# Performance work log

Measured on AMD Instinct MI355X. Metric: run time of the kernel, lower is better.

The kernel has to match this reference:

```python
import jax, jax.numpy as jnp
import numpy as np

CHANNELS = 256
CODEBOOK_SIZE = 8192
UPDATE_SPEED = 0.01
N_TOKENS = 32768


def setup_inputs() -> dict:
    key = jax.random.key(0)
    k1, k2 = jax.random.split(key)
    embeddings = jax.random.normal(k1, (N_TOKENS, CHANNELS), dtype=jnp.float32)
    code_usage = jnp.ones((CODEBOOK_SIZE,), dtype=jnp.float32)
    code_embedding_sum = jax.random.normal(k2, (CODEBOOK_SIZE, CHANNELS), dtype=jnp.float32)
    return {"embeddings": embeddings, "code_usage": code_usage,
            "code_embedding_sum": code_embedding_sum}


def reference(embeddings, code_usage, code_embedding_sum):
    # codebook from EMA statistics: [K, C]
    codebook = code_embedding_sum / jnp.clip(code_usage, 1e-5, None)[:, None]

    # encode: nearest code by Euclidean distance. argmin over codes is
    # invariant under sqrt, so use squared distances (avoids sqrt of [K, N]).
    cb_sq = jnp.sum(codebook * codebook, axis=-1)            # [K]
    x_sq = jnp.sum(embeddings * embeddings, axis=-1)         # [N]
    # d2[k, n] = ||cb_k - x_n||^2
    d2 = cb_sq[:, None] - 2.0 * jnp.einsum('kc,nc->kn', codebook, embeddings) + x_sq[None, :]
    codes = jnp.argmin(d2, axis=0).astype(jnp.int32)         # [N]

    # decode: gather codebook rows
    quantized = jnp.take(codebook, codes, axis=0)            # [N, C]

    # straight-through estimator
    embeddings_q = embeddings + jax.lax.stop_gradient(quantized - embeddings)

    # commitment loss: mse(stop_grad(embeddings_q), embeddings)
    diff = jax.lax.stop_gradient(embeddings_q) - embeddings
    commitment_loss = jnp.mean(diff * diff)

    # EMA updates (training mode, under no_grad in the original)
    n = embeddings.shape[0]
    counts = jax.ops.segment_sum(jnp.ones((n,), dtype=code_usage.dtype),
                                 codes, num_segments=CODEBOOK_SIZE)
    emb_sum = jax.ops.segment_sum(embeddings, codes, num_segments=CODEBOOK_SIZE)
    s = jnp.float32(UPDATE_SPEED)
    new_code_usage = jax.lax.stop_gradient(code_usage * (1.0 - s) + counts * s)
    new_code_embedding_sum = jax.lax.stop_gradient(
        code_embedding_sum * (1.0 - s) + emb_sum * s)

    return codes, embeddings_q, commitment_loss, new_code_usage, new_code_embedding_sum
```

## Files before the change

### kernel.cpp

```cpp
#include <hip/hip_runtime.h>

#define CH 256
#define KC 8192
#define NT 32768

#define TPW 32
#define JT  64
#define JTS 64

typedef _Float16 half4_t __attribute__((ext_vector_type(4)));
typedef _Float16 half8_t __attribute__((ext_vector_type(8)));
typedef float floatx16 __attribute__((ext_vector_type(16)));

typedef __attribute__((address_space(1))) const unsigned int guint_t;
typedef __attribute__((address_space(3))) unsigned int luint_t;

__global__ void k_prep(const float* __restrict__ usage,
                       const float* __restrict__ ces,
                       const float* __restrict__ emb,
                       _Float16* __restrict__ cbh,
                       _Float16* __restrict__ cbl,
                       float* __restrict__ cbsq,
                       _Float16* __restrict__ eh,
                       _Float16* __restrict__ el,
                       int* __restrict__ hist,
                       unsigned long long* __restrict__ packed) {
    int b = blockIdx.x, t = threadIdx.x;
    if (b < KC) {
        float uc = fmaxf(usage[b], 1e-5f);
        float v  = ces[b * CH + t];
        float cb = v / uc;
        _Float16 h = (_Float16)cb;
        cbh[b * CH + t] = h;
        cbl[b * CH + t] = (_Float16)(cb - (float)h);

        float p = cb * cb;
        #pragma unroll
        for (int off = 32; off; off >>= 1) p += __shfl_down(p, off);
        __shared__ float ps[4];
        int lane = t & 63, w = t >> 6;
        if (lane == 0) ps[w] = p;
        __syncthreads();
        if (t == 0) cbsq[b] = ps[0] + ps[1] + ps[2] + ps[3];
        if (t == 1) hist[b] = 0;
        int gid = b * CH + t;
        if (gid < NT) packed[gid] = 0xFFFFFFFFFFFFFFFFull;
    } else {
        int i = (b - KC) * 256 + t;
        float4 v = ((const float4*)emb)[i];
        float va[4] = {v.x, v.y, v.z, v.w};
        half4_t h, l;
        #pragma unroll
        for (int q = 0; q < 4; ++q) {
            _Float16 hh = (_Float16)va[q];
            h[q] = hh;
            l[q] = (_Float16)(va[q] - (float)hh);
        }
        ((half4_t*)eh)[i] = h;
        ((half4_t*)el)[i] = l;
    }
}

__launch_bounds__(512, 2)
__global__ void k_argmin(const _Float16* __restrict__ eh,
                         const _Float16* __restrict__ el,
                         const _Float16* __restrict__ cbh,
                         const _Float16* __restrict__ cbl,
                         const float* __restrict__ cbsq,
                         unsigned long long* __restrict__ packed) {
    __shared__ __align__(16) char smB[131072];

    const int t    = threadIdx.x;
    const int lane = t & 63;
    const int wave = t >> 6;
    const int lr32 = lane & 31;
    const int kh   = lane >> 5;

    const int n0w = blockIdx.x * 256 + wave * TPW;
    const int jq  = blockIdx.y * (JTS * JT);

    half8_t aregh[16], aregl[16];
    {
        const size_t rowoff = (size_t)(n0w + lr32) * CH + kh * 8;
        #pragma unroll
        for (int ks = 0; ks < 16; ++ks) {
            aregh[ks] = *(const half8_t*)(eh + rowoff + ks * 16);
            aregl[ks] = *(const half8_t*)(el + rowoff + ks * 16);
        }
    }

    auto dmaB = [&](int buf, int jt) {
        const int jb = jq + jt * JT;
        #pragma unroll
        for (int d = 0; d < 8; ++d) {
            const int p   = wave * 4 + (d >> 1);
            const int ks  = p >> 1;
            const int h   = p & 1;
            const int sub = d & 1;
            const _Float16* src = h ? cbl : cbh;
            const _Float16* g = src + (size_t)(jb + lane) * CH
                              + ks * 16 + sub * 8;
            __builtin_amdgcn_global_load_lds(
                (guint_t*)g,
                (luint_t*)(smB + buf * 65536 + ks * 4096 + h * 2048
                           + sub * 1024),
                16, 0, 0);
        }
    };

    float minv[16];
    int   mini[16];
    #pragma unroll
    for (int e = 0; e < 16; ++e) { minv[e] = 3.402823466e38f; mini[e] = 0; }

    floatx16 acc0, acc1;
    #pragma unroll
    for (int r = 0; r < 16; ++r) { acc0[r] = 0.f; acc1[r] = 0.f; }

    dmaB(0, 0);
    __syncthreads();

    const int lslot = (kh * 64 + lr32) * 16;

    #pragma unroll 1
    for (int jt = 0; jt < JTS; ++jt) {
        const int buf = jt & 1;
        const int jb  = jq + jt * JT;

        if (jt + 1 < JTS) dmaB(buf ^ 1, jt + 1);

        const float csq0 = cbsq[jb + lr32];
        const float csq1 = cbsq[jb + 32 + lr32];

        const char* bbase = smB + buf * 65536 + lslot;
        #pragma unroll
        for (int ks = 0; ks < 16; ++ks) {
            const char* bp = bbase + ks * 4096;
            half8_t fbh0 = *(const half8_t*)(bp);
            half8_t fbh1 = *(const half8_t*)(bp + 512);
            half8_t fbl0 = *(const half8_t*)(bp + 2048);
            half8_t fbl1 = *(const half8_t*)(bp + 2560);
            acc0 = __builtin_amdgcn_mfma_f32_32x32x16_f16(aregh[ks], fbh0, acc0, 0, 0, 0);
            acc1 = __builtin_amdgcn_mfma_f32_32x32x16_f16(aregh[ks], fbh1, acc1, 0, 0, 0);
            acc0 = __builtin_amdgcn_mfma_f32_32x32x16_f16(aregh[ks], fbl0, acc0, 0, 0, 0);
            acc1 = __builtin_amdgcn_mfma_f32_32x32x16_f16(aregh[ks], fbl1, acc1, 0, 0, 0);
            acc0 = __builtin_amdgcn_mfma_f32_32x32x16_f16(aregl[ks], fbh0, acc0, 0, 0, 0);
            acc1 = __builtin_amdgcn_mfma_f32_32x32x16_f16(aregl[ks], fbh1, acc1, 0, 0, 0);
        }

        #pragma unroll
        for (int r = 0; r < 16; ++r) {
            float s0 = csq0 - 2.0f * acc0[r];
            float s1 = csq1 - 2.0f * acc1[r];
            float sv = s0; int si = jb + lr32;
            if (s1 < sv) { sv = s1; si = jb + 32 + lr32; }
            if (sv < minv[r]) { minv[r] = sv; mini[r] = si; }
            acc0[r] = 0.f;
            acc1[r] = 0.f;
        }

        __syncthreads();
    }

    #pragma unroll
    for (int r = 0; r < 16; ++r) {
        float v = minv[r];
        int   x = mini[r];
        #pragma unroll
        for (int m = 1; m <= 16; m <<= 1) {
            float ov = __shfl_xor(v, m, 64);
            int   ox = __shfl_xor(x, m, 64);
            if (ov < v || (ov == v && ox < x)) { v = ov; x = ox; }
        }
        if (lr32 == 0) {
            int tok = n0w + (r & 3) + 8 * (r >> 2) + 4 * kh;
            unsigned sb = __float_as_uint(v);
            sb = (sb & 0x80000000u) ? ~sb : (sb | 0x80000000u);
            unsigned long long key =
                ((unsigned long long)sb << 32) | (unsigned)x;
            atomicMin(&packed[tok], key);
        }
    }
}

__global__ void k_gather(const float* __restrict__ emb,
                         const float* __restrict__ ces,
                         const float* __restrict__ usage,
                         const unsigned long long* __restrict__ packed,
                         float* __restrict__ out_eq,
                         float* __restrict__ codes_f,
                         int* __restrict__ hist,
                         float* __restrict__ partials) {
    int t = threadIdx.x;
    int wave = t >> 6, lane = t & 63;
    int n = blockIdx.x * 4 + wave;
    int k = (int)(packed[n] & 0xFFFFFFFFull);
    float uc = fmaxf(usage[k], 1e-5f);
    int c = lane * 4;

    float4 e = *(const float4*)&emb[(size_t)n * CH + c];
    float4 v = *(const float4*)&ces[(size_t)k * CH + c];
    float ea[4] = {e.x, e.y, e.z, e.w};
    float va[4] = {v.x, v.y, v.z, v.w};
    float eqa[4];
    float p = 0.0f;
    #pragma unroll
    for (int q = 0; q < 4; ++q) {
        float cb = va[q] / uc;
        float eq = ea[q] + (cb - ea[q]);
        eqa[q] = eq;
        float d = eq - ea[q];
        p += d * d;
    }
    *(float4*)&out_eq[(size_t)n * CH + c] =
        (float4){eqa[0], eqa[1], eqa[2], eqa[3]};

    #pragma unroll
    for (int off = 32; off; off >>= 1) p += __shfl_down(p, off);
    __shared__ float ps[4];
    if (lane == 0) {
        ps[wave] = p;
        codes_f[n] = (float)k;
        atomicAdd(&hist[k], 1);
    }
    __syncthreads();
    if (t == 0) partials[blockIdx.x] = ps[0] + ps[1] + ps[2] + ps[3];
}

__global__ void k_scan(const int* __restrict__ hist,
                       int* __restrict__ offs,
                       int* __restrict__ cursor) {
    __shared__ int bs[256];
    int t = threadIdx.x;
    int base = t * 32;
    int loc[32];
    int s = 0;
    #pragma unroll
    for (int i = 0; i < 32; ++i) { loc[i] = s; s += hist[base + i]; }
    int mysum = s;
    bs[t] = s;
    __syncthreads();
    for (int off = 1; off < 256; off <<= 1) {
        int v = (t >= off) ? bs[t - off] : 0;
        __syncthreads();
        bs[t] += v;
        __syncthreads();
    }
    int excl = bs[t] - mysum;
    #pragma unroll
    for (int i = 0; i < 32; ++i) {
        int o = excl + loc[i];
        offs[base + i]   = o;
        cursor[base + i] = o;
    }
}

__global__ void k_scatter(const unsigned long long* __restrict__ packed,
                          int* __restrict__ cursor,
                          int* __restrict__ bucket) {
    int n = blockIdx.x * 256 + threadIdx.x;
    int k = (int)(packed[n] & 0xFFFFFFFFull);
    int pos = atomicAdd(&cursor[k], 1);
    bucket[pos] = n;
}

__global__ void k_ema(const float* __restrict__ emb,
                      const float* __restrict__ ces,
                      const float* __restrict__ usage,
                      const int* __restrict__ hist,
                      const int* __restrict__ offs,
                      const int* __restrict__ bucket,
                      float* __restrict__ out_ces,
                      float* __restrict__ out_usage) {
    const float s = 0.01f;
    const float oms = 1.0f - s;
    int k = blockIdx.x, t = threadIdx.x;
    int start = offs[k], cnt = hist[k];
    float sum = 0.0f;
    #pragma unroll 2
    for (int i = 0; i < cnt; ++i) {
        int n = bucket[start + i];
        sum += emb[(size_t)n * CH + t];
    }
    out_ces[(size_t)k * CH + t] = oms * ces[(size_t)k * CH + t] + s * sum;
    if (t == 0) out_usage[k] = oms * usage[k] + s * (float)cnt;
}

__global__ void k_final(const float* __restrict__ partials,
                        float* __restrict__ out_loss) {
    int t = threadIdx.x;
    float p = 0.0f;
    for (int i = t; i < NT / 4; i += 256) p += partials[i];
    #pragma unroll
    for (int off = 32; off; off >>= 1) p += __shfl_down(p, off);
    __shared__ float ps[4];
    if ((t & 63) == 0) ps[t >> 6] = p;
    __syncthreads();
    if (t == 0)
        out_loss[0] = (ps[0] + ps[1] + ps[2] + ps[3]) * (1.0f / 8388608.0f);
}

extern "C" void kernel_launch(void* const* d_in, const int* in_sizes, int n_in,
                              void* d_out, int out_size, void* d_ws, size_t ws_size,
                              hipStream_t stream) {
    const float* emb   = (const float*)d_in[0];
    const float* usage = (const float*)d_in[1];
    const float* ces   = (const float*)d_in[2];

    float* out      = (float*)d_out;
    float* o_codes  = out;
    float* o_eq     = out + NT;
    float* o_loss   = o_eq + (size_t)NT * CH;
    float* o_usage  = o_loss + 1;
    float* o_ces    = o_usage + KC;

    unsigned long long* packed = (unsigned long long*)d_ws;
    float* cbsq     = (float*)(packed + NT);
    float* partials = cbsq + KC;
    int* hist   = (int*)(partials + NT / 4);
    int* offs   = hist + KC;
    int* cursor = offs + KC;
    int* bucket = cursor + KC;
    _Float16* eh  = (_Float16*)(bucket + NT);
    _Float16* el  = eh + (size_t)NT * CH;
    _Float16* cbh = el + (size_t)NT * CH;
    _Float16* cbl = cbh + (size_t)KC * CH;

    k_prep<<<KC + NT * CH / 1024, 256, 0, stream>>>(
        usage, ces, emb, cbh, cbl, cbsq, eh, el, hist, packed);
    dim3 agrid(NT / 256, 2);
    k_argmin<<<agrid, 512, 0, stream>>>(eh, el, cbh, cbl, cbsq, packed);
    k_gather<<<NT / 4, 256, 0, stream>>>(emb, ces, usage, packed, o_eq,
                                         o_codes, hist, partials);
    k_scan<<<1, 256, 0, stream>>>(hist, offs, cursor);
    k_scatter<<<NT / 256, 256, 0, stream>>>(packed, cursor, bucket);
    k_ema<<<KC, 256, 0, stream>>>(emb, ces, usage, hist, offs, bucket,
                                  o_ces, o_usage);
    k_final<<<1, 256, 0, stream>>>(partials, o_loss);
}
```

Before: 578.8 us.

## Stream low-half codebook fragments from global into registers, halve LDS staging

Only the high-half fp16 codebook tiles are staged through LDS now. The low-half fragments are loaded straight from global memory into registers in a rotating four-deep software pipeline that runs two k-steps ahead and spans tile boundaries. This halves LDS capacity and traffic per block, which could allow more blocks per CU, and overlaps the global loads with the MFMA chain. The cost is uncoalesced-ish per-lane global loads hitting L2, extra VGPR pressure from the prefetch registers, and exposed latency if the prefetch distance is too short.

```diff
diff --git a/kernel.cpp b/kernel.cpp
--- a/kernel.cpp
+++ b/kernel.cpp
@@ -68,7 +68,7 @@
                          const _Float16* __restrict__ cbl,
                          const float* __restrict__ cbsq,
                          unsigned long long* __restrict__ packed) {
-    __shared__ __align__(16) char smB[131072];
+    __shared__ __align__(16) char smB[65536];
 
     const int t    = threadIdx.x;
     const int lane = t & 63;
@@ -92,18 +92,14 @@
     auto dmaB = [&](int buf, int jt) {
         const int jb = jq + jt * JT;
         #pragma unroll
-        for (int d = 0; d < 8; ++d) {
-            const int p   = wave * 4 + (d >> 1);
-            const int ks  = p >> 1;
-            const int h   = p & 1;
+        for (int d = 0; d < 4; ++d) {
+            const int ks  = wave * 2 + (d >> 1);
             const int sub = d & 1;
-            const _Float16* src = h ? cbl : cbh;
-            const _Float16* g = src + (size_t)(jb + lane) * CH
+            const _Float16* g = cbh + (size_t)(jb + lane) * CH
                               + ks * 16 + sub * 8;
             __builtin_amdgcn_global_load_lds(
                 (guint_t*)g,
-                (luint_t*)(smB + buf * 65536 + ks * 4096 + h * 2048
-                           + sub * 1024),
+                (luint_t*)(smB + buf * 32768 + ks * 2048 + sub * 1024),
                 16, 0, 0);
         }
     };
@@ -117,36 +113,63 @@
     #pragma unroll
     for (int r = 0; r < 16; ++r) { acc0[r] = 0.f; acc1[r] = 0.f; }
 
+    half8_t HA0, HA1, HB0, HB1;
+    half8_t LA0, LA1, LB0, LB1, LC0, LC1, LD0, LD1;
+
+#define LO_ISSUE(KS2, JBX, L)                                                \
+    { const _Float16* g_ = cbl + (size_t)((JBX) + lr32) * CH                 \
+                         + (KS2) * 16 + kh * 8;                              \
+      L##0 = *(const half8_t*)g_;                                           \
+      L##1 = *(const half8_t*)(g_ + 32 * CH); }
+
+#define HI_READ(KS1, H)                                                      \
+    { const char* bp_ = bbase + (KS1) * 2048;                                \
+      H##0 = *(const half8_t*)bp_;                                          \
+      H##1 = *(const half8_t*)(bp_ + 512); }
+
+#define MFMA6(KS, H, L)                                                      \
+    acc0 = __builtin_amdgcn_mfma_f32_32x32x16_f16(aregh[KS], H##0, acc0, 0,0,0); \
+    acc1 = __builtin_amdgcn_mfma_f32_32x32x16_f16(aregh[KS], H##1, acc1, 0,0,0); \
+    acc0 = __builtin_amdgcn_mfma_f32_32x32x16_f16(aregh[KS], L##0, acc0, 0,0,0); \
+    acc1 = __builtin_amdgcn_mfma_f32_32x32x16_f16(aregh[KS], L##1, acc1, 0,0,0); \
+    acc0 = __builtin_amdgcn_mfma_f32_32x32x16_f16(aregl[KS], H##0, acc0, 0,0,0); \
+    acc1 = __builtin_amdgcn_mfma_f32_32x32x16_f16(aregl[KS], H##1, acc1, 0,0,0);
+
     dmaB(0, 0);
+    LO_ISSUE(0, jq, LA)
+    LO_ISSUE(1, jq, LB)
     __syncthreads();
-
-    const int lslot = (kh * 64 + lr32) * 16;
 
     #pragma unroll 1
     for (int jt = 0; jt < JTS; ++jt) {
         const int buf = jt & 1;
         const int jb  = jq + jt * JT;
+        const int jb2 = (jt + 1 < JTS) ? jb + JT : jb;
 
         if (jt + 1 < JTS) dmaB(buf ^ 1, jt + 1);
 
         const float csq0 = cbsq[jb + lr32];
         const float csq1 = cbsq[jb + 32 + lr32];
 
-        const char* bbase = smB + buf * 65536 + lslot;
-        #pragma unroll
-        for (int ks = 0; ks < 16; ++ks) {
-            const char* bp = bbase + ks * 4096;
-            half8_t fbh0 = *(const half8_t*)(bp);
-            half8_t fbh1 = *(const half8_t*)(bp + 512);
-            half8_t fbl0 = *(const half8_t*)(bp + 2048);
-            half8_t fbl1 = *(const half8_t*)(bp + 2560);
-            acc0 = __builtin_amdgcn_mfma_f32_32x32x16_f16(aregh[ks], fbh0, acc0, 0, 0, 0);
-            acc1 = __builtin_amdgcn_mfma_f32_32x32x16_f16(aregh[ks], fbh1, acc1, 0, 0, 0);
-            acc0 = __builtin_amdgcn_mfma_f32_32x32x16_f16(aregh[ks], fbl0, acc0, 0, 0, 0);
-            acc1 = __builtin_amdgcn_mfma_f32_32x32x16_f16(aregh[ks], fbl1, acc1, 0, 0, 0);
-            acc0 = __builtin_amdgcn_mfma_f32_32x32x16_f16(aregl[ks], fbh0, acc0, 0, 0, 0);
-            acc1 = __builtin_amdgcn_mfma_f32_32x32x16_f16(aregl[ks], fbh1, acc1, 0, 0, 0);
-        }
+        const char* bbase = smB + buf * 32768 + kh * 1024 + lr32 * 16;
+
+        HI_READ(0, HA)
+        LO_ISSUE(2,  jb,  LC) HI_READ(1,  HB) MFMA6(0,  HA, LA)
+        LO_ISSUE(3,  jb,  LD) HI_READ(2,  HA) MFMA6(1,  HB, LB)
+        LO_ISSUE(4,  jb,  LA) HI_READ(3,  HB) MFMA6(2,  HA, LC)
+        LO_ISSUE(5,  jb,  LB) HI_READ(4,  HA) MFMA6(3,  HB, LD)
+        LO_ISSUE(6,  jb,  LC) HI_READ(5,  HB) MFMA6(4,  HA, LA)
+        LO_ISSUE(7,  jb,  LD) HI_READ(6,  HA) MFMA6(5,  HB, LB)
+        LO_ISSUE(8,  jb,  LA) HI_READ(7,  HB) MFMA6(6,  HA, LC)
+        LO_ISSUE(9,  jb,  LB) HI_READ(8,  HA) MFMA6(7,  HB, LD)
+        LO_ISSUE(10, jb,  LC) HI_READ(9,  HB) MFMA6(8,  HA, LA)
+        LO_ISSUE(11, jb,  LD) HI_READ(10, HA) MFMA6(9,  HB, LB)
+        LO_ISSUE(12, jb,  LA) HI_READ(11, HB) MFMA6(10, HA, LC)
+        LO_ISSUE(13, jb,  LB) HI_READ(12, HA) MFMA6(11, HB, LD)
+        LO_ISSUE(14, jb,  LC) HI_READ(13, HB) MFMA6(12, HA, LA)
+        LO_ISSUE(15, jb,  LD) HI_READ(14, HA) MFMA6(13, HB, LB)
+        LO_ISSUE(0,  jb2, LA) HI_READ(15, HB) MFMA6(14, HA, LC)
+        LO_ISSUE(1,  jb2, LB)                 MFMA6(15, HB, LD)
 
         #pragma unroll
         for (int r = 0; r < 16; ++r) {
@@ -161,6 +184,9 @@
 
         __syncthreads();
     }
+#undef MFMA6
+#undef HI_READ
+#undef LO_ISSUE
 
     #pragma unroll
     for (int r = 0; r < 16; ++r) {
```

New measurement: 751.4 us. +29.8%, slower.

## Give each wave 64 tokens with 2x2 MFMA tiles and double-buffered LDS fragments

Applied to the files above, without the earlier changes.

The argmin kernel now runs 4 waves of 256 threads, each owning 64 tokens instead of 32. Every codebook fragment read from LDS therefore feeds twice as many MFMAs, which halves LDS read traffic per FLOP. The inner k-loop is hand-unrolled so the next step's B fragments are loaded into registers while the current MFMAs run. In exchange the kernel holds twice as many A registers and accumulators, so occupancy drops to one block per CU and spills become possible.

```diff
diff --git a/kernel.cpp b/kernel.cpp
--- a/kernel.cpp
+++ b/kernel.cpp
@@ -4,7 +4,7 @@
 #define KC 8192
 #define NT 32768
 
-#define TPW 32
+#define TPW 64
 #define JT  64
 #define JTS 64
 
@@ -61,7 +61,7 @@
     }
 }
 
-__launch_bounds__(512, 2)
+__launch_bounds__(256, 1)
 __global__ void k_argmin(const _Float16* __restrict__ eh,
                          const _Float16* __restrict__ el,
                          const _Float16* __restrict__ cbh,
@@ -79,21 +79,24 @@
     const int n0w = blockIdx.x * 256 + wave * TPW;
     const int jq  = blockIdx.y * (JTS * JT);
 
-    half8_t aregh[16], aregl[16];
+    half8_t a0h[16], a0l[16], a1h[16], a1l[16];
     {
-        const size_t rowoff = (size_t)(n0w + lr32) * CH + kh * 8;
+        const size_t ro0 = (size_t)(n0w + lr32) * CH + kh * 8;
+        const size_t ro1 = ro0 + (size_t)32 * CH;
         #pragma unroll
         for (int ks = 0; ks < 16; ++ks) {
-            aregh[ks] = *(const half8_t*)(eh + rowoff + ks * 16);
-            aregl[ks] = *(const half8_t*)(el + rowoff + ks * 16);
+            a0h[ks] = *(const half8_t*)(eh + ro0 + ks * 16);
+            a0l[ks] = *(const half8_t*)(el + ro0 + ks * 16);
+            a1h[ks] = *(const half8_t*)(eh + ro1 + ks * 16);
+            a1l[ks] = *(const half8_t*)(el + ro1 + ks * 16);
         }
     }
 
     auto dmaB = [&](int buf, int jt) {
         const int jb = jq + jt * JT;
         #pragma unroll
-        for (int d = 0; d < 8; ++d) {
-            const int p   = wave * 4 + (d >> 1);
+        for (int d = 0; d < 16; ++d) {
+            const int p   = wave * 8 + (d >> 1);
             const int ks  = p >> 1;
             const int h   = p & 1;
             const int sub = d & 1;
@@ -108,19 +111,46 @@
         }
     };
 
-    float minv[16];
-    int   mini[16];
-    #pragma unroll
-    for (int e = 0; e < 16; ++e) { minv[e] = 3.402823466e38f; mini[e] = 0; }
-
-    floatx16 acc0, acc1;
-    #pragma unroll
-    for (int r = 0; r < 16; ++r) { acc0[r] = 0.f; acc1[r] = 0.f; }
+    float minv[32];
+    int   mini[32];
+    #pragma unroll
+    for (int e = 0; e < 32; ++e) { minv[e] = 3.402823466e38f; mini[e] = 0; }
+
+    floatx16 acc00, acc01, acc10, acc11;
+    #pragma unroll
+    for (int r = 0; r < 16; ++r) {
+        acc00[r] = 0.f; acc01[r] = 0.f; acc10[r] = 0.f; acc11[r] = 0.f;
+    }
 
     dmaB(0, 0);
     __syncthreads();
 
     const int lslot = (kh * 64 + lr32) * 16;
+
+#define PRIME(KS, R)                                                         \
+    { const char* bp_ = bbase + (KS) * 4096;                                 \
+      R##0 = *(const half8_t*)(bp_);                                         \
+      R##1 = *(const half8_t*)(bp_ + 512);                                   \
+      R##2 = *(const half8_t*)(bp_ + 2048);                                  \
+      R##3 = *(const half8_t*)(bp_ + 2560); }
+
+#define MFMA12(KS, B)                                                        \
+    acc00 = __builtin_amdgcn_mfma_f32_32x32x16_f16(a0h[KS], B##0, acc00, 0,0,0); \
+    acc01 = __builtin_amdgcn_mfma_f32_32x32x16_f16(a0h[KS], B##1, acc01, 0,0,0); \
+    acc10 = __builtin_amdgcn_mfma_f32_32x32x16_f16(a1h[KS], B##0, acc10, 0,0,0); \
+    acc11 = __builtin_amdgcn_mfma_f32_32x32x16_f16(a1h[KS], B##1, acc11, 0,0,0); \
+    acc00 = __builtin_amdgcn_mfma_f32_32x32x16_f16(a0h[KS], B##2, acc00, 0,0,0); \
+    acc01 = __builtin_amdgcn_mfma_f32_32x32x16_f16(a0h[KS], B##3, acc01, 0,0,0); \
+    acc10 = __builtin_amdgcn_mfma_f32_32x32x16_f16(a1h[KS], B##2, acc10, 0,0,0); \
+    acc11 = __builtin_amdgcn_mfma_f32_32x32x16_f16(a1h[KS], B##3, acc11, 0,0,0); \
+    acc00 = __builtin_amdgcn_mfma_f32_32x32x16_f16(a0l[KS], B##0, acc00, 0,0,0); \
+    acc01 = __builtin_amdgcn_mfma_f32_32x32x16_f16(a0l[KS], B##1, acc01, 0,0,0); \
+    acc10 = __builtin_amdgcn_mfma_f32_32x32x16_f16(a1l[KS], B##0, acc10, 0,0,0); \
+    acc11 = __builtin_amdgcn_mfma_f32_32x32x16_f16(a1l[KS], B##1, acc11, 0,0,0);
+
+#define STEP(KS, CUR, NXT, LAST)                                             \
+    { if (!(LAST)) PRIME((KS) + 1, NXT)                                      \
+      MFMA12((KS), CUR) }
 
     #pragma unroll 1
     for (int jt = 0; jt < JTS; ++jt) {
@@ -133,39 +163,48 @@
         const float csq1 = cbsq[jb + 32 + lr32];
 
         const char* bbase = smB + buf * 65536 + lslot;
-        #pragma unroll
-        for (int ks = 0; ks < 16; ++ks) {
-            const char* bp = bbase + ks * 4096;
-            half8_t fbh0 = *(const half8_t*)(bp);
-            half8_t fbh1 = *(const half8_t*)(bp + 512);
-            half8_t fbl0 = *(const half8_t*)(bp + 2048);
-            half8_t fbl1 = *(const half8_t*)(bp + 2560);
-            acc0 = __builtin_amdgcn_mfma_f32_32x32x16_f16(aregh[ks], fbh0, acc0, 0, 0, 0);
-            acc1 = __builtin_amdgcn_mfma_f32_32x32x16_f16(aregh[ks], fbh1, acc1, 0, 0, 0);
-            acc0 = __builtin_amdgcn_mfma_f32_32x32x16_f16(aregh[ks], fbl0, acc0, 0, 0, 0);
-            acc1 = __builtin_amdgcn_mfma_f32_32x32x16_f16(aregh[ks], fbl1, acc1, 0, 0, 0);
-            acc0 = __builtin_amdgcn_mfma_f32_32x32x16_f16(aregl[ks], fbh0, acc0, 0, 0, 0);
-            acc1 = __builtin_amdgcn_mfma_f32_32x32x16_f16(aregl[ks], fbh1, acc1, 0, 0, 0);
-        }
+        half8_t p0, p1, p2, p3, q0, q1, q2, q3;
+
+        PRIME(0, p)
+        STEP(0,  p, q, 0) STEP(1,  q, p, 0)
+        STEP(2,  p, q, 0) STEP(3,  q, p, 0)
+        STEP(4,  p, q, 0) STEP(5,  q, p, 0)
+        STEP(6,  p, q, 0) STEP(7,  q, p, 0)
+        STEP(8,  p, q, 0) STEP(9,  q, p, 0)
+        STEP(10, p, q, 0) STEP(11, q, p, 0)
+        STEP(12, p, q, 0) STEP(13, q, p, 0)
+        STEP(14, p, q, 0) STEP(15, q, p, 1)
 
         #pragma unroll
         for (int r = 0; r < 16; ++r) {
-            float s0 = csq0 - 2.0f * acc0[r];
-            float s1 = csq1 - 2.0f * acc1[r];
-            float sv = s0; int si = jb + lr32;
-            if (s1 < sv) { sv = s1; si = jb + 32 + lr32; }
-            if (sv < minv[r]) { minv[r] = sv; mini[r] = si; }
-            acc0[r] = 0.f;
-            acc1[r] = 0.f;
+            {
+                float s0 = csq0 - 2.0f * acc00[r];
+                float s1 = csq1 - 2.0f * acc01[r];
+                float sv = s0; int si = jb + lr32;
+                if (s1 < sv) { sv = s1; si = jb + 32 + lr32; }
+                if (sv < minv[r]) { minv[r] = sv; mini[r] = si; }
+                acc00[r] = 0.f; acc01[r] = 0.f;
+            }
+            {
+                float s0 = csq0 - 2.0f * acc10[r];
+                float s1 = csq1 - 2.0f * acc11[r];
+                float sv = s0; int si = jb + lr32;
+                if (s1 < sv) { sv = s1; si = jb + 32 + lr32; }
+                if (sv < minv[16 + r]) { minv[16 + r] = sv; mini[16 + r] = si; }
+                acc10[r] = 0.f; acc11[r] = 0.f;
+            }
         }
 
         __syncthreads();
     }
-
-    #pragma unroll
-    for (int r = 0; r < 16; ++r) {
-        float v = minv[r];
-        int   x = mini[r];
+#undef STEP
+#undef MFMA12
+#undef PRIME
+
+    #pragma unroll
+    for (int e = 0; e < 32; ++e) {
+        float v = minv[e];
+        int   x = mini[e];
         #pragma unroll
         for (int m = 1; m <= 16; m <<= 1) {
             float ov = __shfl_xor(v, m, 64);
@@ -173,7 +212,8 @@
             if (ov < v || (ov == v && ox < x)) { v = ov; x = ox; }
         }
         if (lr32 == 0) {
-            int tok = n0w + (r & 3) + 8 * (r >> 2) + 4 * kh;
+            const int m = e >> 4, r = e & 15;
+            int tok = n0w + m * 32 + (r & 3) + 8 * (r >> 2) + 4 * kh;
             unsigned sb = __float_as_uint(v);
             sb = (sb & 0x80000000u) ? ~sb : (sb | 0x80000000u);
             unsigned long long key =
@@ -329,7 +369,7 @@
     k_prep<<<KC + NT * CH / 1024, 256, 0, stream>>>(
         usage, ces, emb, cbh, cbl, cbsq, eh, el, hist, packed);
     dim3 agrid(NT / 256, 2);
-    k_argmin<<<agrid, 512, 0, stream>>>(eh, el, cbh, cbl, cbsq, packed);
+    k_argmin<<<agrid, 256, 0, stream>>>(eh, el, cbh, cbl, cbsq, packed);
     k_gather<<<NT / 4, 256, 0, stream>>>(emb, ces, usage, packed, o_eq,
                                          o_codes, hist, partials);
     k_scan<<<1, 256, 0, stream>>>(hist, offs, cursor);
```

After: 649.1 us. +12.1%, slower.
